# Kernel optimization log

Hardware: AMD Instinct MI355X
Metric: run time of the kernel (lower is better)

## Reference

```python
import jax, jax.numpy as jnp
import numpy as np
from jax import lax

BN_EPS = 1e-5

def setup_inputs() -> dict:
    key = jax.random.key(0)
    ks = jax.random.split(key, 4)
    b, C, h, w, dim = 8, 4, 16, 16, 512
    H = 8  # num_heads
    x = jax.random.normal(ks[0], (b, C, h, w, dim), dtype=jnp.float32)
    qkv_w = jax.random.normal(ks[1], (3 * dim, dim), dtype=jnp.float32) * 0.02
    proj_w = jax.random.normal(ks[2], (dim, dim), dtype=jnp.float32) * 0.02
    proj_b = jnp.zeros((dim,), dtype=jnp.float32)
    conv_w = jax.random.normal(ks[3], (H, H, 3, 3), dtype=jnp.float32) * 0.1
    conv_b = jnp.zeros((H,), dtype=jnp.float32)
    bn_gamma = jnp.ones((H,), dtype=jnp.float32)
    bn_beta = jnp.zeros((H,), dtype=jnp.float32)
    bn_mean = jnp.zeros((H,), dtype=jnp.float32)
    bn_var = jnp.ones((H,), dtype=jnp.float32)
    return {"x": x, "qkv_w": qkv_w, "proj_w": proj_w, "proj_b": proj_b,
            "conv_w": conv_w, "conv_b": conv_b, "bn_gamma": bn_gamma,
            "bn_beta": bn_beta, "bn_mean": bn_mean, "bn_var": bn_var}


def reference(x, qkv_w, proj_w, proj_b, conv_w, conv_b, bn_gamma, bn_beta, bn_mean, bn_var):
    b, C, h, w, c = x.shape
    n = C * h * w
    H = conv_w.shape[0]            # num_heads
    hd = c // H                    # head_dim
    scale = hd ** (-0.5)

    x2 = x.reshape(b, n, c)
    qkv = x2 @ qkv_w.T             # [b, n, 3c]
    qkv = qkv.reshape(b, n, 3, H, hd)
    q = qkv[:, :, 0].transpose(0, 2, 1, 3)  # [b, H, n, hd]
    k = qkv[:, :, 1].transpose(0, 2, 1, 3)
    v = qkv[:, :, 2].transpose(0, 2, 1, 3)

    attn = jnp.einsum('bhnd,bhmd->bhnm', q * scale, k)  # [b, H, n, n]

    # dwc2: Conv2d(H->H, 3x3, pad=1) + BatchNorm2d (eval) + Sigmoid on the score matrix
    attn = lax.conv_general_dilated(attn, conv_w, (1, 1), 'SAME',
                                    dimension_numbers=('NCHW', 'OIHW', 'NCHW'))
    attn = attn + conv_b[None, :, None, None]
    inv = bn_gamma * lax.rsqrt(bn_var + BN_EPS)
    attn = attn * inv[None, :, None, None] + (bn_beta - bn_mean * inv)[None, :, None, None]
    attn = jax.nn.sigmoid(attn)

    attn = jax.nn.softmax(attn, axis=-1)
    z = jnp.einsum('bhnm,bhmd->bhnd', attn, v)           # [b, H, n, hd]
    z = z.transpose(0, 2, 1, 3).reshape(b, n, c)
    z = z @ proj_w.T + proj_b
    out = z.reshape(b, C, h, w, c) + x
    return out
```

## Files before the change

kernel.cpp:

```cpp
#include <hip/hip_runtime.h>


#define DINL __device__ __forceinline__
typedef unsigned short u16;
typedef unsigned int u32;
typedef unsigned long long u64;
typedef short bf16x8 __attribute__((ext_vector_type(8)));
typedef float f32x4 __attribute__((ext_vector_type(4)));

DINL u16 f2bf(float f) {
  u32 u = __float_as_uint(f);
  u += 0x7fffu + ((u >> 16) & 1u);
  return (u16)(u >> 16);
}
DINL float bflo(u32 u) { return __uint_as_float(u << 16); }
DINL float bfhi(u32 u) { return __uint_as_float(u & 0xffff0000u); }
DINL u32 cvtpk_bf16(float lo, float hi) {
  u32 r;
  asm("v_cvt_pk_bf16_f32 %0, %1, %2" : "=v"(r) : "v"(lo), "v"(hi));
  return r;
}
DINL u32 pk4_fp8(float a, float b, float c, float d) {
  u32 r = 0;
  r = (u32)__builtin_amdgcn_cvt_pk_fp8_f32(a, b, (int)r, false);
  r = (u32)__builtin_amdgcn_cvt_pk_fp8_f32(c, d, (int)r, true);
  return r;
}
DINL unsigned char f2fp8(float v) {
  return (unsigned char)((u32)__builtin_amdgcn_cvt_pk_fp8_f32(v, v, 0, false) & 0xffu);
}

__global__ __launch_bounds__(256) void k_cvt_xw(const float* __restrict__ x,
                                                const float* __restrict__ qw,
                                                u16* __restrict__ Xb,
                                                u16* __restrict__ QWb) {
  int gid = blockIdx.x * 256 + threadIdx.x;
  int stride = gridDim.x * 256;
  for (int i = gid; i < 622592; i += stride) {
    const float* src;
    u16* dst;
    size_t off;
    if (i < 524288) { src = x; dst = Xb; off = (size_t)i * 8; }
    else { src = qw; dst = QWb; off = (size_t)(i - 524288) * 8; }
    float4 a = *(const float4*)&src[off];
    float4 b = *(const float4*)&src[off + 4];
    uint4 p;
    p.x = cvtpk_bf16(a.x, a.y); p.y = cvtpk_bf16(a.z, a.w);
    p.z = cvtpk_bf16(b.x, b.y); p.w = cvtpk_bf16(b.z, b.w);
    *(uint4*)&dst[off] = p;
  }
}

__global__ __launch_bounds__(256) void k_prep(
    const float* __restrict__ cw, const float* __restrict__ cb,
    const float* __restrict__ bg, const float* __restrict__ bb,
    const float* __restrict__ bm, const float* __restrict__ bv,
    const float* __restrict__ proj_w, unsigned char* __restrict__ wbake,
    float* __restrict__ bbake, u16* __restrict__ PWb) {
  const int blk = blockIdx.x, tid = threadIdx.x;
  if (blk == 0) {
    for (int u = tid; u < 1536; u += 256) {
      int tap = u >> 9, rem2 = u & 511;
      int m = rem2 >> 5, kk = rem2 & 31;
      int p = m >> 3, oh = m & 7;
      int ih = kk >> 2, rr = kk & 3;
      int dr = rr - p;
      float v = 0.f;
      if (dr >= 0 && dr < 3) {
        float ah = bg[oh] * rsqrtf(bv[oh] + 1e-5f);
        v = cw[((oh * 8 + ih) * 3 + dr) * 3 + tap] * ah;
      }
      wbake[tap * 640 + m * 40 + kk] = f2fp8(v);
    }
    if (tid < 8) {
      float ah = bg[tid] * rsqrtf(bv[tid] + 1e-5f);
      bbake[tid] = cb[tid] * ah + bb[tid] - bm[tid] * ah;
    }
  } else {
    int i = (blk - 1) * 256 + tid;
    float4 a = *(const float4*)&proj_w[(size_t)i * 8];
    float4 b = *(const float4*)&proj_w[(size_t)i * 8 + 4];
    uint4 p;
    p.x = cvtpk_bf16(a.x, a.y); p.y = cvtpk_bf16(a.z, a.w);
    p.z = cvtpk_bf16(b.x, b.y); p.w = cvtpk_bf16(b.z, b.w);
    *(uint4*)&PWb[(size_t)i * 8] = p;
  }
}

__global__ __launch_bounds__(256) void k_qkv(const u16* __restrict__ xb,
                                             const u16* __restrict__ wb,
                                             u16* __restrict__ Q,
                                             u16* __restrict__ K,
                                             u16* __restrict__ V) {
  __shared__ __align__(16) u16 sA[128 * 64];
  __shared__ __align__(16) u16 sB[128 * 64];
  const int tid = threadIdx.x;
  const int m0 = blockIdx.x * 128, n0 = blockIdx.y * 128;
  const int lane = tid & 63, wid = tid >> 6;
  const int wr = wid >> 1, wc = wid & 1;
  const int l15 = lane & 15, l4 = lane >> 4;
  const int row = tid >> 1, half = tid & 1, xr = row & 7;
  f32x4 acc[4][4] = {};
  for (int k0 = 0; k0 < 512; k0 += 64) {
    __syncthreads();
    {
      const u16* ga = &xb[(size_t)(m0 + row) * 512 + k0 + half * 32];
      const u16* gb = &wb[(size_t)(n0 + row) * 512 + k0 + half * 32];
#pragma unroll
      for (int q = 0; q < 4; ++q) {
        int gp = (half * 4 + q) ^ xr;
        *(uint4*)&sA[row * 64 + gp * 8] = *(const uint4*)&ga[q * 8];
        *(uint4*)&sB[row * 64 + gp * 8] = *(const uint4*)&gb[q * 8];
      }
    }
    __syncthreads();
#pragma unroll
    for (int ks = 0; ks < 2; ++ks) {
      bf16x8 af[4], bfr[4];
#pragma unroll
      for (int mr = 0; mr < 4; ++mr) {
        int rr = wr * 64 + mr * 16 + l15;
        af[mr] = *(bf16x8*)&sA[rr * 64 + ((ks * 4 + l4) ^ (rr & 7)) * 8];
      }
#pragma unroll
      for (int nr = 0; nr < 4; ++nr) {
        int rr = wc * 64 + nr * 16 + l15;
        bfr[nr] = *(bf16x8*)&sB[rr * 64 + ((ks * 4 + l4) ^ (rr & 7)) * 8];
      }
#pragma unroll
      for (int mr = 0; mr < 4; ++mr)
#pragma unroll
        for (int nr = 0; nr < 4; ++nr)
          acc[mr][nr] = __builtin_amdgcn_mfma_f32_16x16x32_bf16(af[mr], bfr[nr],
                                                                acc[mr][nr], 0, 0, 0);
    }
  }
#pragma unroll
  for (int nr = 0; nr < 4; ++nr) {
    int nn = n0 + wc * 64 + nr * 16 + l15;
    int which = nn >> 9, co = nn & 511;
    int head = co >> 6, d = co & 63;
    u16* dst = (which == 0) ? Q : (which == 1) ? K : V;
    float sc = (which == 0) ? 0.125f : 1.f;
#pragma unroll
    for (int mr = 0; mr < 4; ++mr) {
      int mb = m0 + wr * 64 + mr * 16 + l4 * 4;
#pragma unroll
      for (int r = 0; r < 4; ++r) {
        int m = mb + r;
        int bb = m >> 10, ii = m & 1023;
        dst[((((size_t)bb * 8 + head) << 10) + ii) * 64 + d] =
            f2bf(acc[mr][nr][r] * sc);
      }
    }
  }
}

__global__ __launch_bounds__(256) void k_qk(const u16* __restrict__ Q,
                                            const u16* __restrict__ Kp,
                                            unsigned char* __restrict__ S8) {
  const int bh = blockIdx.z;
  const u16* Qb = Q + (size_t)bh * 65536;
  const u16* Kb = Kp + (size_t)bh * 65536;
  __shared__ __align__(16) u16 sQ[128 * 64];
  __shared__ __align__(16) u16 sK[128 * 64];
  const int tid = threadIdx.x;
  const int m0 = blockIdx.x * 128, n0 = blockIdx.y * 128;
  {
    int row = tid >> 1, half = tid & 1;
    const u16* gq = &Qb[(size_t)(m0 + row) * 64 + half * 32];
    const u16* gk = &Kb[(size_t)(n0 + row) * 64 + half * 32];
    int xr = row & 7;
#pragma unroll
    for (int q = 0; q < 4; ++q) {
      int gp = (half * 4 + q) ^ xr;
      *(uint4*)&sQ[row * 64 + gp * 8] = *(const uint4*)&gq[q * 8];
      *(uint4*)&sK[row * 64 + gp * 8] = *(const uint4*)&gk[q * 8];
    }
  }
  __syncthreads();
  const int lane = tid & 63, wid = tid >> 6;
  const int wr = wid >> 1, wc = wid & 1;
  const int l15 = lane & 15, l4 = lane >> 4;
  f32x4 acc[4][4] = {};
  bf16x8 af[4][2], bf[4][2];
#pragma unroll
  for (int mr = 0; mr < 4; ++mr) {
    int row = wr * 64 + mr * 16 + l15;
#pragma unroll
    for (int ks = 0; ks < 2; ++ks)
      af[mr][ks] = *(bf16x8*)&sQ[row * 64 + ((ks * 4 + l4) ^ (row & 7)) * 8];
  }
#pragma unroll
  for (int nr = 0; nr < 4; ++nr) {
    int row = wc * 64 + nr * 16 + l15;
#pragma unroll
    for (int ks = 0; ks < 2; ++ks)
      bf[nr][ks] = *(bf16x8*)&sK[row * 64 + ((ks * 4 + l4) ^ (row & 7)) * 8];
  }
#pragma unroll
  for (int mr = 0; mr < 4; ++mr)
#pragma unroll
    for (int nr = 0; nr < 4; ++nr)
#pragma unroll
      for (int ks = 0; ks < 2; ++ks)
        acc[mr][nr] = __builtin_amdgcn_mfma_f32_16x16x32_bf16(af[mr][ks], bf[nr][ks],
                                                              acc[mr][nr], 0, 0, 0);
  __syncthreads();
  unsigned char* t8 = (unsigned char*)sQ;
#pragma unroll
  for (int mr = 0; mr < 4; ++mr) {
    int mloc = wr * 64 + mr * 16 + l4 * 4;
#pragma unroll
    for (int nr = 0; nr < 4; ++nr) {
      int nloc = wc * 64 + nr * 16 + l15;
#pragma unroll
      for (int r = 0; r < 4; ++r)
        t8[(mloc + r) * 128 + nloc] = f2fp8(acc[mr][nr][r]);
    }
  }
  __syncthreads();
  {
    int row = tid >> 1, c0 = (tid & 1) * 64;
    unsigned char* dst = &S8[((size_t)bh << 20) + (size_t)(m0 + row) * 1024 + n0 + c0];
#pragma unroll
    for (int q = 0; q < 4; ++q)
      *(uint4*)&dst[q * 16] = *(uint4*)&t8[row * 128 + c0 + q * 16];
  }
}

__global__ __launch_bounds__(256) void k_conv(
    const unsigned char* __restrict__ S8, unsigned char* __restrict__ P8,
    float* __restrict__ Dbuf, const unsigned char* __restrict__ wbake,
    const float* __restrict__ bbake) {
  const int blk = blockIdx.x;
  const int b = blk >> 10;
  const int rem = blk & 1023;
  const int ip = rem >> 1, jh = rem & 1;
  const int i0 = ip * 2, j0 = jh * 512;
  __shared__ __align__(16) unsigned char sC[514 * 40];
  __shared__ __align__(16) unsigned char sA[3][16][40];
  __shared__ float sRedD[4][16];
  const int tid = threadIdx.x;
  const int lane = tid & 63, wid = tid >> 6;
  const int l15 = lane & 15, l4 = lane >> 4;

  if (tid < 120) ((uint4*)sA)[tid] = ((const uint4*)wbake)[tid];
  if (tid >= 120 && tid < 136) {
    int t = tid - 120;
    int side = t & 1, ih = t >> 1;
    int g = side ? (j0 + 512) : (j0 - 1);
    u32 v = 0;
    if (g >= 0 && g < 1024) {
      const unsigned char* Sb = S8 + (((size_t)(b * 8 + ih)) << 20);
#pragma unroll
      for (int rr = 0; rr < 4; ++rr) {
        int r = i0 - 1 + rr;
        u32 byte = (r >= 0 && r < 1024) ? (u32)Sb[(size_t)r * 1024 + g] : 0u;
        v |= byte << (8 * rr);
      }
    }
    *(u32*)&sC[(side ? 513 : 0) * 40 + ih * 4] = v;
  }
  {
    const int ihs = tid >> 5;
    const int lc = tid & 31;
    const unsigned char* p1 =
        S8 + (((size_t)(b * 8 + ihs)) << 20) + (size_t)i0 * 1024 + j0 + lc * 4;
    const bool intr = (i0 != 0) && (i0 != 1022);
#pragma unroll
    for (int it = 0; it < 4; ++it) {
      const unsigned char* pp = p1 + it * 128;
      u32 w0, w3;
      u32 w1 = *(const u32*)pp;
      u32 w2 = *(const u32*)(pp + 1024);
      if (intr) {
        w0 = *(const u32*)(pp - 1024);
        w3 = *(const u32*)(pp + 2048);
      } else {
        w0 = (i0 != 0) ? *(const u32*)(pp - 1024) : 0u;
        w3 = (i0 != 1022) ? *(const u32*)(pp + 2048) : 0u;
      }
      u32 p01l = __builtin_amdgcn_perm(w1, w0, 0x05010400u);
      u32 p23l = __builtin_amdgcn_perm(w3, w2, 0x05010400u);
      u32 p01h = __builtin_amdgcn_perm(w1, w0, 0x07030602u);
      u32 p23h = __builtin_amdgcn_perm(w3, w2, 0x07030602u);
      unsigned char* dst = &sC[(lc * 4 + it * 128 + 1) * 40 + ihs * 4];
      *(u32*)(dst + 0)   = __builtin_amdgcn_perm(p23l, p01l, 0x05040100u);
      *(u32*)(dst + 40)  = __builtin_amdgcn_perm(p23l, p01l, 0x07060302u);
      *(u32*)(dst + 80)  = __builtin_amdgcn_perm(p23h, p01h, 0x05040100u);
      *(u32*)(dst + 120) = __builtin_amdgcn_perm(p23h, p01h, 0x07060302u);
    }
  }
  __syncthreads();

  long wfr[3];
#pragma unroll
  for (int tap = 0; tap < 3; ++tap)
    wfr[tap] = *(long*)&sA[tap][l15][l4 * 8];
  const int oh = l15 & 7, p = l15 >> 3;
  const float biasm = bbake[oh];
  const int jw = wid * 128;
  unsigned char* Pst = &P8[((size_t)(b * 8 + oh) << 20) + ((size_t)(i0 + p) << 10) +
                           j0 + jw + l4 * 4];
  const unsigned char* sCb = &sC[(size_t)(jw + l15) * 40 + l4 * 8];
  float dsum = 0.f;

  for (int t = 0; t < 8; ++t) {
    f32x4 acc = {0.f, 0.f, 0.f, 0.f};
#pragma unroll
    for (int tap = 0; tap < 3; ++tap) {
      long sfr = *(long*)(sCb + t * 640 + tap * 40);
      acc = __builtin_amdgcn_mfma_f32_16x16x32_fp8_fp8(sfr, wfr[tap], acc, 0, 0, 0);
    }
    float e[4];
#pragma unroll
    for (int r = 0; r < 4; ++r) {
      float tt = acc[r] + biasm;
      float sg = 1.f / (1.f + __expf(-tt));
      e[r] = __expf(sg);
    }
    *(u32*)(Pst + t * 16) = pk4_fp8(e[0], e[1], e[2], e[3]);
    dsum += (e[0] + e[1]) + (e[2] + e[3]);
  }
  dsum += __shfl_xor(dsum, 16);
  dsum += __shfl_xor(dsum, 32);
  if (l4 == 0) sRedD[wid][l15] = dsum;
  __syncthreads();
  if (tid < 16) {
    int pp = tid >> 3, ohh = tid & 7;
    Dbuf[(size_t)jh * 65536 + ((size_t)(b * 8 + ohh) << 10) + i0 + pp] =
        sRedD[0][tid] + sRedD[1][tid] + sRedD[2][tid] + sRedD[3][tid];
  }
}

__global__ __launch_bounds__(256) void k_av(const unsigned char* __restrict__ P8,
                                            const u16* __restrict__ V,
                                            const float* __restrict__ Dbuf,
                                            u16* __restrict__ Z) {
  const int bh = blockIdx.y, m0 = blockIdx.x * 128;
  const int b = bh >> 3, h = bh & 7;
  __shared__ __align__(16) unsigned char sA8[128 * 64];
  __shared__ __align__(16) unsigned char sVt[64 * 64];
  const int tid = threadIdx.x, lane = tid & 63, wid = tid >> 6;
  const int wr = wid >> 1, wc = wid & 1, l15 = lane & 15, l4 = lane >> 4;
  f32x4 acc[4][2] = {};
  for (int k0 = 0; k0 < 1024; k0 += 64) {
    __syncthreads();
    {
      int row = tid >> 1, c0 = (tid & 1) * 32;
      const unsigned char* src =
          &P8[((size_t)bh << 20) + (size_t)(m0 + row) * 1024 + k0 + c0];
      uint4 a0 = *(const uint4*)src, a1 = *(const uint4*)(src + 16);
      u64 ul[4];
      ul[0] = (u64)a0.x | ((u64)a0.y << 32);
      ul[1] = (u64)a0.z | ((u64)a0.w << 32);
      ul[2] = (u64)a1.x | ((u64)a1.y << 32);
      ul[3] = (u64)a1.z | ((u64)a1.w << 32);
      int xr = row & 7, gb = c0 >> 3;
#pragma unroll
      for (int t = 0; t < 4; ++t)
        *(u64*)&sA8[row * 64 + ((gb + t) ^ xr) * 8] = ul[t];
    }
    {
      int j = tid >> 2, d0 = (tid & 3) * 16;
      const u16* src = &V[((size_t)bh << 16) + (size_t)(k0 + j) * 64 + d0];
      uint4 v0 = *(const uint4*)src, v1 = *(const uint4*)(src + 16);
      u32 wv[8] = {v0.x, v0.y, v0.z, v0.w, v1.x, v1.y, v1.z, v1.w};
#pragma unroll
      for (int t = 0; t < 8; ++t) {
        u32 p = (u32)__builtin_amdgcn_cvt_pk_fp8_f32(bflo(wv[t]), bfhi(wv[t]), 0, false);
        int da = d0 + t * 2, db = da + 1;
        sVt[da * 64 + (((j >> 3) ^ (da & 7)) << 3) + (j & 7)] = (unsigned char)(p & 0xff);
        sVt[db * 64 + (((j >> 3) ^ (db & 7)) << 3) + (j & 7)] = (unsigned char)((p >> 8) & 0xff);
      }
    }
    __syncthreads();
    long bfr[2][2];
#pragma unroll
    for (int nr = 0; nr < 2; ++nr) {
      int row = wc * 32 + nr * 16 + l15;
#pragma unroll
      for (int ks = 0; ks < 2; ++ks)
        bfr[nr][ks] = *(long*)&sVt[row * 64 + (((ks * 4 + l4) ^ (row & 7)) << 3)];
    }
#pragma unroll
    for (int mr = 0; mr < 4; ++mr) {
      int row = wr * 64 + mr * 16 + l15;
      long afr[2];
#pragma unroll
      for (int ks = 0; ks < 2; ++ks)
        afr[ks] = *(long*)&sA8[row * 64 + (((ks * 4 + l4) ^ (row & 7)) << 3)];
#pragma unroll
      for (int nr = 0; nr < 2; ++nr)
#pragma unroll
        for (int ks = 0; ks < 2; ++ks)
          acc[mr][nr] = __builtin_amdgcn_mfma_f32_16x16x32_fp8_fp8(afr[ks], bfr[nr][ks],
                                                                   acc[mr][nr], 0, 0, 0);
    }
  }
#pragma unroll
  for (int mr = 0; mr < 4; ++mr) {
    int mbase = m0 + wr * 64 + mr * 16 + l4 * 4;
    float dv[4];
#pragma unroll
    for (int r = 0; r < 4; ++r) {
      size_t di = ((size_t)bh << 10) + mbase + r;
      dv[r] = 1.f / (Dbuf[di] + Dbuf[di + 65536]);
    }
#pragma unroll
    for (int nr = 0; nr < 2; ++nr) {
      int d = wc * 32 + nr * 16 + l15;
#pragma unroll
      for (int r = 0; r < 4; ++r)
        Z[((size_t)(b * 1024 + mbase + r)) * 512 + h * 64 + d] =
            f2bf(acc[mr][nr][r] * dv[r]);
    }
  }
}

__global__ __launch_bounds__(256) void k_proj(const u16* __restrict__ Z,
                                              const u16* __restrict__ wb,
                                              const float* __restrict__ bias,
                                              const float* __restrict__ xin,
                                              float* __restrict__ out) {
  __shared__ __align__(16) u16 sA[128 * 64];
  __shared__ __align__(16) u16 sB[128 * 64];
  const int tid = threadIdx.x;
  const int m0 = blockIdx.x * 128, n0 = blockIdx.y * 128;
  const int lane = tid & 63, wid = tid >> 6;
  const int wr = wid >> 1, wc = wid & 1;
  const int l15 = lane & 15, l4 = lane >> 4;
  const int row = tid >> 1, half = tid & 1, xr = row & 7;
  f32x4 acc[4][4] = {};
  for (int k0 = 0; k0 < 512; k0 += 64) {
    __syncthreads();
    {
      const u16* gz = &Z[(size_t)(m0 + row) * 512 + k0 + half * 32];
      const u16* gb = &wb[(size_t)(n0 + row) * 512 + k0 + half * 32];
#pragma unroll
      for (int q = 0; q < 4; ++q) {
        int gp = (half * 4 + q) ^ xr;
        *(uint4*)&sA[row * 64 + gp * 8] = *(const uint4*)&gz[q * 8];
        *(uint4*)&sB[row * 64 + gp * 8] = *(const uint4*)&gb[q * 8];
      }
    }
    __syncthreads();
#pragma unroll
    for (int ks = 0; ks < 2; ++ks) {
      bf16x8 af[4], bfr[4];
#pragma unroll
      for (int mr = 0; mr < 4; ++mr) {
        int rr = wr * 64 + mr * 16 + l15;
        af[mr] = *(bf16x8*)&sA[rr * 64 + ((ks * 4 + l4) ^ (rr & 7)) * 8];
      }
#pragma unroll
      for (int nr = 0; nr < 4; ++nr) {
        int rr = wc * 64 + nr * 16 + l15;
        bfr[nr] = *(bf16x8*)&sB[rr * 64 + ((ks * 4 + l4) ^ (rr & 7)) * 8];
      }
#pragma unroll
      for (int mr = 0; mr < 4; ++mr)
#pragma unroll
        for (int nr = 0; nr < 4; ++nr)
          acc[mr][nr] = __builtin_amdgcn_mfma_f32_16x16x32_bf16(af[mr], bfr[nr],
                                                                acc[mr][nr], 0, 0, 0);
    }
  }
#pragma unroll
  for (int nr = 0; nr < 4; ++nr) {
    int nn = n0 + wc * 64 + nr * 16 + l15;
    float bv2 = bias[nn];
#pragma unroll
    for (int mr = 0; mr < 4; ++mr) {
      int mb = m0 + wr * 64 + mr * 16 + l4 * 4;
#pragma unroll
      for (int r = 0; r < 4; ++r) {
        size_t o = (size_t)(mb + r) * 512 + nn;
        out[o] = acc[mr][nr][r] + bv2 + xin[o];
      }
    }
  }
}

extern "C" void kernel_launch(void* const* d_in, const int* in_sizes, int n_in,
                              void* d_out, int out_size, void* d_ws, size_t ws_size,
                              hipStream_t stream) {
  const size_t need = 160ull << 20;
  if (ws_size < need) return;

  const float* x      = (const float*)d_in[0];
  const float* qkv_w  = (const float*)d_in[1];
  const float* proj_w = (const float*)d_in[2];
  const float* proj_b = (const float*)d_in[3];
  const float* conv_w = (const float*)d_in[4];
  const float* conv_b = (const float*)d_in[5];
  const float* bn_g   = (const float*)d_in[6];
  const float* bn_b   = (const float*)d_in[7];
  const float* bn_m   = (const float*)d_in[8];
  const float* bn_v   = (const float*)d_in[9];
  float* out = (float*)d_out;

  char* W = (char*)d_ws;
  u16* Wq = (u16*)W;
  float* Dbuf = (float*)W;
  u16* PWb = (u16*)(W + (1ull << 20));
  unsigned char* wbake = (unsigned char*)(W + (2ull << 20));
  float* bbake = (float*)(W + (2ull << 20) + 4096);
  u16* Wk = (u16*)(W + (8ull << 20));
  u16* Wv = (u16*)(W + (16ull << 20));
  u16* Wz = (u16*)(W + (24ull << 20));
  unsigned char* S8 = (unsigned char*)(W + (32ull << 20));
  u16* Xb = (u16*)S8;
  u16* QWb = (u16*)(W + (40ull << 20));
  unsigned char* P8 = (unsigned char*)(W + (96ull << 20));

  k_cvt_xw<<<2048, 256, 0, stream>>>(x, qkv_w, Xb, QWb);
  k_qkv<<<dim3(64, 12), 256, 0, stream>>>(Xb, QWb, Wq, Wk, Wv);
  k_qk<<<dim3(8, 8, 64), 256, 0, stream>>>(Wq, Wk, S8);
  k_prep<<<129, 256, 0, stream>>>(conv_w, conv_b, bn_g, bn_b, bn_m, bn_v,
                                  proj_w, wbake, bbake, PWb);
  k_conv<<<dim3(8192), 256, 0, stream>>>(S8, P8, Dbuf, wbake, bbake);
  k_av<<<dim3(8, 64), 256, 0, stream>>>(P8, Wv, Dbuf, Wz);
  k_proj<<<dim3(64, 4), 256, 0, stream>>>(Wz, PWb, proj_b, x, out);
}
```

Baseline: 162.1 us.

## Emit V pre-transposed in fp8 from QKV GEMM and widen conv halo loads

```diff
diff --git a/kernel.cpp b/kernel.cpp
--- a/kernel.cpp
+++ b/kernel.cpp
@@ -13,8 +13,6 @@
   u += 0x7fffu + ((u >> 16) & 1u);
   return (u16)(u >> 16);
 }
-DINL float bflo(u32 u) { return __uint_as_float(u << 16); }
-DINL float bfhi(u32 u) { return __uint_as_float(u & 0xffff0000u); }
 DINL u32 cvtpk_bf16(float lo, float hi) {
   u32 r;
   asm("v_cvt_pk_bf16_f32 %0, %1, %2" : "=v"(r) : "v"(lo), "v"(hi));
@@ -91,7 +89,7 @@
                                              const u16* __restrict__ wb,
                                              u16* __restrict__ Q,
                                              u16* __restrict__ K,
-                                             u16* __restrict__ V) {
+                                             unsigned char* __restrict__ Vt8) {
   __shared__ __align__(16) u16 sA[128 * 64];
   __shared__ __align__(16) u16 sB[128 * 64];
   const int tid = threadIdx.x;
@@ -135,22 +133,40 @@
                                                                 acc[mr][nr], 0, 0, 0);
     }
   }
-#pragma unroll
-  for (int nr = 0; nr < 4; ++nr) {
-    int nn = n0 + wc * 64 + nr * 16 + l15;
-    int which = nn >> 9, co = nn & 511;
-    int head = co >> 6, d = co & 63;
-    u16* dst = (which == 0) ? Q : (which == 1) ? K : V;
-    float sc = (which == 0) ? 0.125f : 1.f;
-#pragma unroll
-    for (int mr = 0; mr < 4; ++mr) {
-      int mb = m0 + wr * 64 + mr * 16 + l4 * 4;
-#pragma unroll
-      for (int r = 0; r < 4; ++r) {
-        int m = mb + r;
-        int bb = m >> 10, ii = m & 1023;
-        dst[((((size_t)bb * 8 + head) << 10) + ii) * 64 + d] =
-            f2bf(acc[mr][nr][r] * sc);
+  const int which0 = n0 >> 9;
+  if (which0 == 2) {
+#pragma unroll
+    for (int nr = 0; nr < 4; ++nr) {
+      int nn = n0 + wc * 64 + nr * 16 + l15;
+      int co = nn & 511;
+      int head = co >> 6, d = co & 63;
+#pragma unroll
+      for (int mr = 0; mr < 4; ++mr) {
+        int mb = m0 + wr * 64 + mr * 16 + l4 * 4;
+        int bb = mb >> 10, ii = mb & 1023;
+        u32 pw = pk4_fp8(acc[mr][nr][0], acc[mr][nr][1], acc[mr][nr][2],
+                         acc[mr][nr][3]);
+        *(u32*)&Vt8[(((size_t)(bb * 8 + head)) << 16) + (size_t)d * 1024 + ii] = pw;
+      }
+    }
+  } else {
+#pragma unroll
+    for (int nr = 0; nr < 4; ++nr) {
+      int nn = n0 + wc * 64 + nr * 16 + l15;
+      int co = nn & 511;
+      int head = co >> 6, d = co & 63;
+      u16* dst = (which0 == 0) ? Q : K;
+      float sc = (which0 == 0) ? 0.125f : 1.f;
+#pragma unroll
+      for (int mr = 0; mr < 4; ++mr) {
+        int mb = m0 + wr * 64 + mr * 16 + l4 * 4;
+#pragma unroll
+        for (int r = 0; r < 4; ++r) {
+          int m = mb + r;
+          int bb = m >> 10, ii = m & 1023;
+          dst[((((size_t)bb * 8 + head) << 10) + ii) * 64 + d] =
+              f2bf(acc[mr][nr][r] * sc);
+        }
       }
     }
   }
@@ -266,26 +282,23 @@
     const int ihs = tid >> 5;
     const int lc = tid & 31;
     const unsigned char* p1 =
-        S8 + (((size_t)(b * 8 + ihs)) << 20) + (size_t)i0 * 1024 + j0 + lc * 4;
-    const bool intr = (i0 != 0) && (i0 != 1022);
-#pragma unroll
-    for (int it = 0; it < 4; ++it) {
-      const unsigned char* pp = p1 + it * 128;
-      u32 w0, w3;
-      u32 w1 = *(const u32*)pp;
-      u32 w2 = *(const u32*)(pp + 1024);
-      if (intr) {
-        w0 = *(const u32*)(pp - 1024);
-        w3 = *(const u32*)(pp + 2048);
-      } else {
-        w0 = (i0 != 0) ? *(const u32*)(pp - 1024) : 0u;
-        w3 = (i0 != 1022) ? *(const u32*)(pp + 2048) : 0u;
-      }
-      u32 p01l = __builtin_amdgcn_perm(w1, w0, 0x05010400u);
-      u32 p23l = __builtin_amdgcn_perm(w3, w2, 0x05010400u);
-      u32 p01h = __builtin_amdgcn_perm(w1, w0, 0x07030602u);
-      u32 p23h = __builtin_amdgcn_perm(w3, w2, 0x07030602u);
-      unsigned char* dst = &sC[(lc * 4 + it * 128 + 1) * 40 + ihs * 4];
+        S8 + (((size_t)(b * 8 + ihs)) << 20) + (size_t)i0 * 1024 + j0 + lc * 16;
+    uint4 r1 = *(const uint4*)p1;
+    uint4 r2 = *(const uint4*)(p1 + 1024);
+    uint4 r0 = make_uint4(0, 0, 0, 0), r3 = make_uint4(0, 0, 0, 0);
+    if (i0 != 0) r0 = *(const uint4*)(p1 - 1024);
+    if (i0 != 1022) r3 = *(const uint4*)(p1 + 2048);
+    u32 w0s[4] = {r0.x, r0.y, r0.z, r0.w};
+    u32 w1s[4] = {r1.x, r1.y, r1.z, r1.w};
+    u32 w2s[4] = {r2.x, r2.y, r2.z, r2.w};
+    u32 w3s[4] = {r3.x, r3.y, r3.z, r3.w};
+#pragma unroll
+    for (int g = 0; g < 4; ++g) {
+      u32 p01l = __builtin_amdgcn_perm(w1s[g], w0s[g], 0x05010400u);
+      u32 p23l = __builtin_amdgcn_perm(w3s[g], w2s[g], 0x05010400u);
+      u32 p01h = __builtin_amdgcn_perm(w1s[g], w0s[g], 0x07030602u);
+      u32 p23h = __builtin_amdgcn_perm(w3s[g], w2s[g], 0x07030602u);
+      unsigned char* dst = &sC[(lc * 16 + g * 4 + 1) * 40 + ihs * 4];
       *(u32*)(dst + 0)   = __builtin_amdgcn_perm(p23l, p01l, 0x05040100u);
       *(u32*)(dst + 40)  = __builtin_amdgcn_perm(p23l, p01l, 0x07060302u);
       *(u32*)(dst + 80)  = __builtin_amdgcn_perm(p23h, p01h, 0x05040100u);
@@ -335,7 +348,7 @@
 }
 
 __global__ __launch_bounds__(256) void k_av(const unsigned char* __restrict__ P8,
-                                            const u16* __restrict__ V,
+                                            const unsigned char* __restrict__ Vt8,
                                             const float* __restrict__ Dbuf,
                                             u16* __restrict__ Z) {
   const int bh = blockIdx.y, m0 = blockIdx.x * 128;
@@ -344,6 +357,7 @@
   __shared__ __align__(16) unsigned char sVt[64 * 64];
   const int tid = threadIdx.x, lane = tid & 63, wid = tid >> 6;
   const int wr = wid >> 1, wc = wid & 1, l15 = lane & 15, l4 = lane >> 4;
+  const int vd = tid >> 2, vj = (tid & 3) * 16;
   f32x4 acc[4][2] = {};
   for (int k0 = 0; k0 < 1024; k0 += 64) {
     __syncthreads();
@@ -363,17 +377,12 @@
         *(u64*)&sA8[row * 64 + ((gb + t) ^ xr) * 8] = ul[t];
     }
     {
-      int j = tid >> 2, d0 = (tid & 3) * 16;
-      const u16* src = &V[((size_t)bh << 16) + (size_t)(k0 + j) * 64 + d0];
-      uint4 v0 = *(const uint4*)src, v1 = *(const uint4*)(src + 16);
-      u32 wv[8] = {v0.x, v0.y, v0.z, v0.w, v1.x, v1.y, v1.z, v1.w};
-#pragma unroll
-      for (int t = 0; t < 8; ++t) {
-        u32 p = (u32)__builtin_amdgcn_cvt_pk_fp8_f32(bflo(wv[t]), bfhi(wv[t]), 0, false);
-        int da = d0 + t * 2, db = da + 1;
-        sVt[da * 64 + (((j >> 3) ^ (da & 7)) << 3) + (j & 7)] = (unsigned char)(p & 0xff);
-        sVt[db * 64 + (((j >> 3) ^ (db & 7)) << 3) + (j & 7)] = (unsigned char)((p >> 8) & 0xff);
-      }
+      uint4 v = *(const uint4*)&Vt8[((size_t)bh << 16) + (size_t)vd * 1024 + k0 + vj];
+      u64 lo = (u64)v.x | ((u64)v.y << 32);
+      u64 hi = (u64)v.z | ((u64)v.w << 32);
+      int g0 = vj >> 3, xd = vd & 7;
+      *(u64*)&sVt[vd * 64 + ((g0 ^ xd) << 3)] = lo;
+      *(u64*)&sVt[vd * 64 + (((g0 + 1) ^ xd) << 3)] = hi;
     }
     __syncthreads();
     long bfr[2][2];
@@ -508,7 +517,7 @@
   unsigned char* wbake = (unsigned char*)(W + (2ull << 20));
   float* bbake = (float*)(W + (2ull << 20) + 4096);
   u16* Wk = (u16*)(W + (8ull << 20));
-  u16* Wv = (u16*)(W + (16ull << 20));
+  unsigned char* Vt8 = (unsigned char*)(W + (16ull << 20));
   u16* Wz = (u16*)(W + (24ull << 20));
   unsigned char* S8 = (unsigned char*)(W + (32ull << 20));
   u16* Xb = (u16*)S8;
@@ -516,11 +525,11 @@
   unsigned char* P8 = (unsigned char*)(W + (96ull << 20));
 
   k_cvt_xw<<<2048, 256, 0, stream>>>(x, qkv_w, Xb, QWb);
-  k_qkv<<<dim3(64, 12), 256, 0, stream>>>(Xb, QWb, Wq, Wk, Wv);
+  k_qkv<<<dim3(64, 12), 256, 0, stream>>>(Xb, QWb, Wq, Wk, Vt8);
   k_qk<<<dim3(8, 8, 64), 256, 0, stream>>>(Wq, Wk, S8);
   k_prep<<<129, 256, 0, stream>>>(conv_w, conv_b, bn_g, bn_b, bn_m, bn_v,
                                   proj_w, wbake, bbake, PWb);
   k_conv<<<dim3(8192), 256, 0, stream>>>(S8, P8, Dbuf, wbake, bbake);
-  k_av<<<dim3(8, 64), 256, 0, stream>>>(P8, Wv, Dbuf, Wz);
+  k_av<<<dim3(8, 64), 256, 0, stream>>>(P8, Vt8, Dbuf, Wz);
   k_proj<<<dim3(64, 4), 256, 0, stream>>>(Wz, PWb, proj_b, x, out);
 }
```

Result: slower. 183.7 us (+13.3%).
